# Performance work log

Measured on AMD Instinct MI355X. Metric: run time of the kernel, lower is better.

Reference implementation:

```python
import jax, jax.numpy as jnp
import numpy as np
import math

B, CIN, COUT, K, G, SD, H = 8, 512, 512, 3, 16, 512, 32
EPS = 1e-8


def _blur_kernel():
    k = jnp.array([1., 3., 3., 1.], dtype=jnp.float32)
    k = k[None, :] * k[:, None]
    k = k / k.sum()
    return k * 4.0  # upsample_factor ** 2


def setup_inputs() -> dict:
    key = jax.random.key(0)
    ks = jax.random.split(key, 10)
    return {
        "x": jax.random.normal(ks[0], (B, CIN, H, H), jnp.float32),
        "co": jax.random.uniform(ks[1], (1, CIN, CIN), jnp.float32),
        "style": jax.random.normal(ks[2], (B, 2 * SD), jnp.float32),
        "noise": jax.random.normal(ks[3], (B, 1, 2 * H, 2 * H), jnp.float32),
        "W": jax.random.normal(ks[4], (1, COUT, CIN, K, K), jnp.float32),
        "mb_w": jax.random.normal(ks[5], (G, SD), jnp.float32),
        "mb_b": jnp.ones((G,), jnp.float32),
        "mod_w": jax.random.normal(ks[6], (CIN, SD), jnp.float32),
        "mod_b": jnp.ones((CIN,), jnp.float32),
        "cluster": jax.random.normal(ks[7], (G, CIN), jnp.float32),
        "gate": -jnp.ones((1,), jnp.float32),
        "tmpr": -2.0 * jnp.ones((1,), jnp.float32),
        "noise_weight": jnp.zeros((1,), jnp.float32),
        "flr_bias": jnp.zeros((COUT,), jnp.float32),
    }


def _l2norm(x, axis):
    n = jnp.linalg.norm(x, axis=axis, keepdims=True)
    return x / jnp.maximum(n, 1e-12)


def reference(x, co, style, noise, W, mb_w, mb_b, mod_w, mod_b,
              cluster, gate, tmpr, noise_weight, flr_bias):
    scale = 1.0 / math.sqrt(CIN * K * K)   # GroupModulatedConv2d.scale
    lin_scale = 1.0 / math.sqrt(SD)        # EqualLinear scale (lr_mul=1)

    t = jax.nn.sigmoid(tmpr) * 5.0
    g = jax.nn.sigmoid(gate)
    S = jax.nn.sigmoid((co - g) * 50.0)                    # (1,Cin,Cin)
    cl = jax.nn.softmax(t * cluster, axis=0)               # (G,Cin)
    loss1 = jnp.sum((cl.T @ cl - jax.lax.stop_gradient(S)) ** 2)
    loss2 = jnp.sum((jnp.float32(CIN * CIN / G) - jnp.sum(S)) ** 2)
    grouped = jax.lax.stop_gradient(jnp.round(jax.nn.softmax(cl * 500.0, axis=0))) + 1e-6

    s1, s2 = style[:, :SD], style[:, SD:]
    style_base = (s1 @ (mb_w * lin_scale).T + mb_b)[:, :, None]   # (B,G,1)
    st = (s2 @ (mod_w * lin_scale).T + mod_b)[:, None, :]         # (B,1,Cin)
    tmp = _l2norm(grouped[None] * st, axis=2)                     # (B,G,Cin)
    st = jnp.sum(tmp * style_base, axis=1)                        # (B,Cin)

    w = scale * W * st[:, None, :, None, None]                    # (B,Cout,Cin,K,K)
    demod = jax.lax.rsqrt(jnp.sum(w * w, axis=(2, 3, 4)) + EPS)   # (B,Cout)
    w = w * demod[:, :, None, None, None]

    # conv_transpose2d(stride=2, pad=0, groups=B) == per-sample conv with
    # lhs_dilation=2, padding=K-1, spatially-flipped kernel.
    wf = w[:, :, :, ::-1, ::-1]

    def per_sample(xi, wi):  # xi (Cin,h,w), wi (Cout,Cin,K,K)
        return jax.lax.conv_general_dilated(
            xi[None], wi, window_strides=(1, 1),
            padding=((K - 1, K - 1), (K - 1, K - 1)), lhs_dilation=(2, 2),
            dimension_numbers=('NCHW', 'OIHW', 'NCHW'))[0]

    out = jax.vmap(per_sample)(x, wf)                             # (B,Cout,65,65)

    # Blur: upfirdn2d, pad=(1,1), depthwise 4x4 symmetric FIR kernel.
    bk = _blur_kernel()
    kdw = jnp.broadcast_to(bk[None, None], (COUT, 1, 4, 4))
    out = jax.lax.conv_general_dilated(
        out, kdw, (1, 1), ((1, 1), (1, 1)), feature_group_count=COUT,
        dimension_numbers=('NCHW', 'OIHW', 'NCHW'))                # (B,Cout,64,64)

    # Correlation of base weights (detached, fed to next layer as `co`).
    wflat = W.reshape(COUT, -1)
    wn = _l2norm(wflat, axis=1)
    co_out = jax.lax.stop_gradient((wn @ wn.T)[None])              # (1,Cout,Cout)

    # NoiseInjection + FusedLeakyReLU
    out = out + noise_weight * noise
    out = jax.nn.leaky_relu(out + flr_bias[None, :, None, None], 0.2) * math.sqrt(2.0)
    return out, co_out, loss1, loss2
```

## Files before the change

kernel.cpp:

```cpp
#include <hip/hip_runtime.h>
#include <hip/hip_bf16.h>

#define NB 8
#define LIN_SCALE 0.044194173824159216f
#define SCALE 0.014731391274719736f

typedef __attribute__((ext_vector_type(8))) short short8;
typedef __attribute__((ext_vector_type(4))) float floatx4;

static constexpr size_t O_XS   = 0;
static constexpr size_t O_OUT1 = 9469952;
static constexpr size_t O_WRT  = 44081152;
static constexpr size_t O_WB   = 48799744;
static constexpr size_t O_PG   = 53518336;
static constexpr size_t O_WSQ  = 61906944;
static constexpr size_t O_CL   = 62955520;
static constexpr size_t O_GR   = O_CL + 32768;
static constexpr size_t O_SB   = O_GR + 32768;
static constexpr size_t O_ST0  = O_SB + 1024;
static constexpr size_t O_STS  = O_ST0 + 16384;
static constexpr size_t O_ST2  = O_STS + 16384;
static constexpr size_t O_WNI  = O_ST2 + 16384;
static constexpr size_t O_DM   = O_WNI + 2048;
static constexpr size_t O_ACC  = O_DM + 16384;

static constexpr size_t OUT_CO = 16777216;
static constexpr size_t OUT_L  = 17039360;

__device__ const int c_ylim[4] = {33,33,32,32};
__device__ const int c_xlim[4] = {33,32,33,32};
__device__ const int c_ntap[4] = {4,2,2,1};
__device__ const int c_tap0[4] = {0,4,6,8};
__device__ const int c_nmb[4]  = {69,66,66,64};
__device__ const int c_cnt[4]  = {276,264,264,256};
__device__ const int c_dy[9] = {-1,-1,0,0, -1,0, 0,0, 0};
__device__ const int c_dx[9] = {-1,0,-1,0, 0,0, -1,0, 0};
__device__ const int c_ky[9] = {2,2,0,0, 2,0, 1,1, 1};
__device__ const int c_kx[9] = {2,0,2,0, 1,1, 2,0, 1};
__device__ const long c_poff[4] = {0, 4460544, 8785920, 13111296};

__device__ __forceinline__ float wave_red(float v) {
#pragma unroll
  for (int s = 32; s > 0; s >>= 1) v += __shfl_down(v, s);
  return v;
}

__device__ __forceinline__ void gl_lds16(const void* g, void* l) {
  __builtin_amdgcn_global_load_lds((const __attribute__((address_space(1))) void*)g,
                                   (__attribute__((address_space(3))) void*)l, 16, 0, 0);
}

__device__ __forceinline__ unsigned short bf16b(float f) {
  union { __hip_bfloat16 h; unsigned short u; } cv;
  cv.h = __float2bfloat16(f);
  return cv.u;
}

__device__ __forceinline__ float bfu(unsigned short u) {
  union { float f; unsigned u32; } c; c.u32 = ((unsigned)u) << 16; return c.f;
}

__device__ __forceinline__ int xcd_chunk(int lb, int cnt) {
  const int q = cnt >> 3, r = cnt & 7;
  const int c = lb & 7, i = lb >> 3;
  return (c < r) ? c*(q+1) + i : r*(q+1) + (c - r)*q + i;
}

__global__ __launch_bounds__(256) void k_big1(const float* __restrict__ W,
    float* __restrict__ wsq, float* __restrict__ wni,
    __hip_bfloat16* __restrict__ wrt, unsigned short* __restrict__ wb,
    const float* __restrict__ style, const float* __restrict__ mod_w,
    const float* __restrict__ mod_b, float* __restrict__ st0,
    const float* __restrict__ co, const float* __restrict__ gate,
    const float* __restrict__ cluster, const float* __restrict__ tmpr,
    const float* __restrict__ mb_w, const float* __restrict__ mb_b,
    float* __restrict__ gr, float* __restrict__ sb,
    float* __restrict__ pacc, __hip_bfloat16* __restrict__ xs) {
  __shared__ float sh[8192];
  __shared__ float extra[8];
  const int bid = blockIdx.x, tid = threadIdx.x;
  const int lane = tid & 63, wv = tid >> 6;
  if (bid < 512) {
    const int o = bid;
    for (int j = tid; j < 4608; j += 256) sh[j] = W[(size_t)o*4608 + j];
    __syncthreads();
    float tot = 0.f;
#pragma unroll
    for (int half = 0; half < 2; half++) {
      const int i = tid + half*256;
      float s = 0.f;
#pragma unroll
      for (int k = 0; k < 9; k++) { float w = sh[i*9 + k]; s = fmaf(w, w, s); }
      wsq[o*512 + i] = s; tot += s;
#pragma unroll
      for (int tp = 0; tp < 9; tp++)
        wrt[((size_t)tp*512 + o)*512 + i] = __float2bfloat16(sh[i*9 + c_ky[tp]*3 + c_kx[tp]]);
    }
    for (int j = tid; j < 4608; j += 256) wb[(size_t)o*4608 + j] = bf16b(sh[j]);
    tot = wave_red(tot);
    if (lane == 0) extra[wv] = tot;
    __syncthreads();
    if (tid == 0) wni[o] = 1.f / fmaxf(sqrtf(extra[0]+extra[1]+extra[2]+extra[3]), 1e-12f);
  } else if (bid < 576) {
    const int b = (bid - 512) >> 3, oc = (bid - 512) & 7;
    sh[tid] = style[b*1024 + 512 + tid];
    sh[tid + 256] = style[b*1024 + 768 + tid];
    __syncthreads();
#pragma unroll
    for (int rr = 0; rr < 16; rr++) {
      const int c = oc*64 + wv*16 + rr;
      const float* mw = mod_w + (size_t)c*512;
      float acc = 0.f;
#pragma unroll
      for (int it = 0; it < 8; it++) acc = fmaf(mw[lane + 64*it], sh[lane + 64*it], acc);
      acc = wave_red(acc);
      if (lane == 0) st0[b*512 + c] = acc*LIN_SCALE + mod_b[c];
    }
  } else if (bid < 1088) {
    const int i = bid - 576;
    const float tt = 5.f / (1.f + expf(-tmpr[0]));
    const float gg = 1.f / (1.f + expf(-gate[0]));
    for (int j = tid; j < 512; j += 256) {
      float v[16]; float m = -1e30f;
#pragma unroll
      for (int g = 0; g < 16; g++) { v[g] = tt * cluster[g*512 + j]; m = fmaxf(m, v[g]); }
      float s = 0.f;
#pragma unroll
      for (int g = 0; g < 16; g++) { v[g] = expf(v[g] - m); s += v[g]; }
      float inv = 1.f / s;
#pragma unroll
      for (int g = 0; g < 16; g++) sh[g*512 + j] = v[g] * inv;
    }
    __syncthreads();
    float cli[16];
#pragma unroll
    for (int k = 0; k < 16; k++) cli[k] = sh[k*512 + i];
    float p1 = 0.f, p2 = 0.f;
    for (int j = tid; j < 512; j += 256) {
      float d = 0.f;
#pragma unroll
      for (int k = 0; k < 16; k++) d = fmaf(cli[k], sh[k*512 + j], d);
      float S = 1.f / (1.f + expf(-50.f*(co[i*512 + j] - gg)));
      float e = d - S;
      p1 = fmaf(e, e, p1); p2 += S;
    }
    p1 = wave_red(p1); p2 = wave_red(p2);
    if (lane == 0) { extra[wv] = p1; extra[4 + wv] = p2; }
    __syncthreads();
    if (tid == 0)  pacc[i]       = extra[0]+extra[1]+extra[2]+extra[3];
    if (tid == 64) pacc[512 + i] = extra[4]+extra[5]+extra[6]+extra[7];
  } else if (bid == 1088) {
    const float tt = 5.f / (1.f + expf(-tmpr[0]));
#pragma unroll
    for (int h = 0; h < 2; h++) {
      const int c = tid + h*256;
      float v[16]; float m = -1e30f;
#pragma unroll
      for (int g = 0; g < 16; g++) { v[g] = tt * cluster[g*512 + c]; m = fmaxf(m, v[g]); }
      float s = 0.f;
#pragma unroll
      for (int g = 0; g < 16; g++) { v[g] = expf(v[g] - m); s += v[g]; }
      float inv = 1.f / s;
      float clv[16]; float m2 = -1e30f;
#pragma unroll
      for (int g = 0; g < 16; g++) { clv[g] = v[g]*inv; m2 = fmaxf(m2, 500.f*clv[g]); }
      float s2 = 0.f; float e2[16];
#pragma unroll
      for (int g = 0; g < 16; g++) { e2[g] = expf(500.f*clv[g] - m2); s2 += e2[g]; }
      float i2 = 1.f / s2;
#pragma unroll
      for (int g = 0; g < 16; g++) gr[g*512 + c] = rintf(e2[g]*i2) + 1e-6f;
    }
    for (int task = wv; task < 128; task += 4) {
      int b = task >> 4, g = task & 15;
      const float* s1 = style + b*1024;
      const float* mw = mb_w + g*512;
      float acc = 0.f;
#pragma unroll
      for (int it = 0; it < 8; it++) acc = fmaf(s1[lane + 64*it], mw[lane + 64*it], acc);
      acc = wave_red(acc);
      if (lane == 0) sb[b*16 + g] = acc*LIN_SCALE + mb_b[g];
    }
  } else {
    const int id0 = (bid - 1089)*256 + tid;
    const float4 z = make_float4(0.f, 0.f, 0.f, 0.f);
    float4* xq = (float4*)xs;
#pragma unroll
    for (int it = 0; it < 22; ++it) {
      const int id = id0 + it*3072;
      const int c = id & 63;
      const int pb = id >> 6;
      const int b = pb / 132;
      const int pix = pb - b*132;
      int y, xx;
      if (pix < 34)       { y = 0;        xx = pix; }
      else if (pix < 68)  { y = 33;       xx = pix - 34; }
      else if (pix < 100) { y = pix - 67; xx = 0; }
      else                { y = pix - 99; xx = 33; }
      xq[((size_t)(b*34 + y)*34 + xx)*64 + c] = z;
    }
  }
}

__global__ __launch_bounds__(256) void k_big2(const float* __restrict__ st0,
    const float* __restrict__ gr, const float* __restrict__ sb,
    const float* __restrict__ wsq, float* __restrict__ dm,
    const float* __restrict__ x, __hip_bfloat16* __restrict__ xs,
    const float* __restrict__ pacc, float* __restrict__ out_tail) {
  __shared__ float L[64*65];
  __shared__ float red[16][4];
  __shared__ float inv[16];
  __shared__ float sbb[16];
  const int tid = threadIdx.x;
  const int lane = tid & 63, wv = tid >> 6;

  if (blockIdx.x == 1088) {
    float a = pacc[tid] + pacc[tid + 256];
    float b2 = pacc[512 + tid] + pacc[768 + tid];
    a = wave_red(a); b2 = wave_red(b2);
    if (lane == 0) { red[0][wv] = a; red[1][wv] = b2; }
    __syncthreads();
    if (tid == 0) {
      float p1 = red[0][0]+red[0][1]+red[0][2]+red[0][3];
      float p2 = red[1][0]+red[1][1]+red[1][2]+red[1][3];
      out_tail[0] = p1;
      float d = 16384.f - p2;
      out_tail[1] = d*d;
    }
    return;
  }

  const int b = (blockIdx.x < 64) ? (blockIdx.x >> 3) : ((blockIdx.x - 64) >> 7);
  float s0 = st0[b*512 + tid], s1 = st0[b*512 + 256 + tid];
  float g0[16], g1[16];
#pragma unroll
  for (int g = 0; g < 16; g++) { g0[g] = gr[g*512 + tid]; g1[g] = gr[g*512 + 256 + tid]; }
#pragma unroll
  for (int g = 0; g < 16; g++) {
    float a = g0[g]*s0, c = g1[g]*s1;
    float p = wave_red(a*a + c*c);
    if (lane == 0) red[g][wv] = p;
  }
  if (tid < 16) sbb[tid] = sb[b*16 + tid];
  __syncthreads();
  if (tid < 16) {
    float ttn = red[tid][0] + red[tid][1] + red[tid][2] + red[tid][3];
    inv[tid] = 1.f / fmaxf(sqrtf(ttn), 1e-12f);
  }
  __syncthreads();
  float f0 = 0.f, f1 = 0.f;
#pragma unroll
  for (int g = 0; g < 16; g++) {
    float w = inv[g]*sbb[g];
    f0 = fmaf(g0[g], w, f0); f1 = fmaf(g1[g], w, f1);
  }
  const float sn0 = s0*f0, sn1 = s1*f1;

  if (blockIdx.x < 64) {
    const int oc = blockIdx.x & 7;
    L[tid] = sn0*sn0;
    L[tid + 256] = sn1*sn1;
    __syncthreads();
#pragma unroll
    for (int rr = 0; rr < 16; rr++) {
      const int o = oc*64 + wv*16 + rr;
      const float* wp = wsq + (size_t)o*512;
      float acc = 0.f;
#pragma unroll
      for (int it = 0; it < 8; it++) acc = fmaf(wp[lane + 64*it], L[lane + 64*it], acc);
      acc = wave_red(acc);
      if (lane == 0) dm[b*512 + o] = rsqrtf((1.0f/4608.0f)*acc + 1e-8f);
    }
    return;
  }

  L[tid] = sn0*SCALE;
  L[tid + 256] = sn1*SCALE;
  __syncthreads();
  const int id = blockIdx.x - 64;
  const int p0 = ((id >> 3) & 15) * 64;
  const int i0 = (id & 7) * 64;
  const int iw = tid & 63, pw = tid >> 6;
  const float sv = L[i0 + iw];
  __syncthreads();
  const int lp = tid & 63, li = tid >> 6;
  const float* xp = x + ((size_t)b*512 + i0)*1024 + p0;
#pragma unroll
  for (int ii = 0; ii < 16; ii++) {
    const int i = li + 4*ii;
    L[i*65 + lp] = xp[(size_t)i*1024 + lp];
  }
  __syncthreads();
#pragma unroll
  for (int pp = 0; pp < 16; pp++) {
    const int pix = p0 + pw + 4*pp;
    const int y = pix >> 5, xq = pix & 31;
    xs[(((size_t)b*34 + (y+1))*34 + (xq+1))*512 + i0 + iw] = __float2bfloat16(L[iw*65 + pw + 4*pp] * sv);
  }
}

__global__ __launch_bounds__(256, 4) void k_mfma(
    const __hip_bfloat16* __restrict__ xs, const __hip_bfloat16* __restrict__ wrt,
    __hip_bfloat16* __restrict__ out1, const __hip_bfloat16* __restrict__ wb,
    float* __restrict__ pgram) {
  __shared__ __hip_bfloat16 smem[16384];
  const int fid = blockIdx.x;
  const int tid = threadIdx.x;
  const int lane = tid & 63, wv = tid >> 6;
  const int wm = (wv >> 1) << 6, wn = (wv & 1) << 6;
  const int col16 = lane & 15, quad = lane >> 4;
  const int colp = col16 ^ ((col16 >> 2) & 1);
  const int soff = (quad ^ (col16 & 3)) << 3;

  int aoff[4], boff[4];
#pragma unroll
  for (int t = 0; t < 4; t++) {
    aoff[t] = (wm + t*16 + colp)*32 + soff;
    boff[t] = 4096 + (wn + t*16 + colp)*32 + soff;
  }
  floatx4 acc[4][4];
#pragma unroll
  for (int i = 0; i < 4; i++)
#pragma unroll
    for (int j = 0; j < 4; j++) acc[i][j] = (floatx4){0.f, 0.f, 0.f, 0.f};

  if (fid >= 276 && fid < 404) {
    const int g = xcd_chunk(fid - 276, 128);
    const int m0 = (g & 3) * 128, n0 = ((g >> 2) & 3) * 128;
    const long kz = (long)(g >> 4) * 576;
    long abase[2], bbase[2]; int ldso[2];
#pragma unroll
    for (int r = 0; r < 2; r++) {
      const int idx = r*256 + tid;
      const int rowp = idx >> 2;
      const int row = rowp ^ ((rowp >> 2) & 1);
      const int kc = (((idx & 3) ^ (row & 3)) << 3);
      abase[r] = (long)(m0 + row)*4608 + kz + kc;
      bbase[r] = (long)(n0 + row)*4608 + kz + kc;
      ldso[r] = idx << 3;
    }
#define STAGE_GRAM(s_) do { \
      const int kk_ = (s_) << 5; \
      const int lo_ = ((s_) & 1) << 13; \
      gl_lds16(wb + (abase[0] + kk_), smem + lo_ + ldso[0]); \
      gl_lds16(wb + (abase[1] + kk_), smem + lo_ + ldso[1]); \
      gl_lds16(wb + (bbase[0] + kk_), smem + lo_ + 4096 + ldso[0]); \
      gl_lds16(wb + (bbase[1] + kk_), smem + lo_ + 4096 + ldso[1]); \
    } while (0)
    STAGE_GRAM(0);
    for (int s = 0; s < 18; ++s) {
      if (s + 1 < 18) {
        STAGE_GRAM(s + 1);
        asm volatile("s_waitcnt vmcnt(4)\n\ts_barrier" ::: "memory");
      } else {
        asm volatile("s_waitcnt vmcnt(0)\n\ts_barrier" ::: "memory");
      }
      const int lo = (s & 1) << 13;
      short8 af[4], bfr[4];
#pragma unroll
      for (int t = 0; t < 4; t++) {
        af[t]  = *(const short8*)(smem + lo + aoff[t]);
        bfr[t] = *(const short8*)(smem + lo + boff[t]);
      }
#pragma unroll
      for (int i = 0; i < 4; i++)
#pragma unroll
        for (int j = 0; j < 4; j++)
          acc[i][j] = __builtin_amdgcn_mfma_f32_16x16x32_bf16(af[i], bfr[j], acc[i][j], 0, 0, 0);
      asm volatile("s_barrier" ::: "memory");
    }
    float* pg = pgram + (size_t)(g >> 4) * 262144;
#pragma unroll
    for (int i = 0; i < 4; i++)
#pragma unroll
      for (int j = 0; j < 4; j++) {
        const int m = m0 + wm + i*16 + (quad << 2);
        const int n = n0 + wn + j*16 + col16;
#pragma unroll
        for (int r = 0; r < 4; r++) pg[(size_t)(m + r)*512 + n] = acc[i][j][r];
      }
    return;
  }

  int cls, lb;
  if (fid < 276)      { cls = 0; lb = fid; }
  else if (fid < 668) { cls = 1; lb = fid - 404; }
  else if (fid < 932) { cls = 2; lb = fid - 668; }
  else                { cls = 3; lb = fid - 932; }
  const int lg = xcd_chunk(lb, c_cnt[cls]);
  const int mb = lg >> 2, nb = lg & 3;
  const int xlim = c_xlim[cls];
  const int npix = c_ylim[cls] * xlim;
  const int M = NB * npix;
  const int m0 = mb * 128, n0 = nb * 128;
  const int t0 = c_tap0[cls];
  const int ntap = c_ntap[cls];

  long abase[2], bbase[2]; int ldso[2];
#pragma unroll
  for (int r = 0; r < 2; r++) {
    const int idx = r*256 + tid;
    const int rowp = idx >> 2;
    const int row = rowp ^ ((rowp >> 2) & 1);
    const int kc = (((idx & 3) ^ (row & 3)) << 3);
    int rm = m0 + row; if (rm >= M) rm = 0;
    const int b = rm / npix; const int rem = rm - b*npix;
    const int yy = rem / xlim; const int xx = rem - yy*xlim;
    abase[r] = ((long)(b*34 + yy + 1)*34 + (xx + 1))*512 + kc;
    bbase[r] = ((long)(t0*512 + n0 + row))*512 + kc;
    ldso[r] = idx << 3;
  }

  const int nst = ntap << 4;
#define STAGE_CONV(s_) do { \
    const int tap_ = t0 + ((s_) >> 4); \
    const long adel_ = (long)((c_dy[tap_]*34 + c_dx[tap_])*512); \
    const long bdel_ = (long)((s_) >> 4) << 18; \
    const int kk_ = ((s_) & 15) << 5; \
    const int lo_ = ((s_) & 1) << 13; \
    gl_lds16(xs + (abase[0] + adel_ + kk_), smem + lo_ + ldso[0]); \
    gl_lds16(xs + (abase[1] + adel_ + kk_), smem + lo_ + ldso[1]); \
    gl_lds16(wrt + (bbase[0] + bdel_ + kk_), smem + lo_ + 4096 + ldso[0]); \
    gl_lds16(wrt + (bbase[1] + bdel_ + kk_), smem + lo_ + 4096 + ldso[1]); \
  } while (0)
  STAGE_CONV(0);
  for (int s = 0; s < nst; ++s) {
    if (s + 1 < nst) {
      STAGE_CONV(s + 1);
      asm volatile("s_waitcnt vmcnt(4)\n\ts_barrier" ::: "memory");
    } else {
      asm volatile("s_waitcnt vmcnt(0)\n\ts_barrier" ::: "memory");
    }
    const int lo = (s & 1) << 13;
    short8 af[4], bfr[4];
#pragma unroll
    for (int t = 0; t < 4; t++) {
      af[t]  = *(const short8*)(smem + lo + aoff[t]);
      bfr[t] = *(const short8*)(smem + lo + boff[t]);
    }
#pragma unroll
    for (int i = 0; i < 4; i++)
#pragma unroll
      for (int j = 0; j < 4; j++)
        acc[i][j] = __builtin_amdgcn_mfma_f32_16x16x32_bf16(af[i], bfr[j], acc[i][j], 0, 0, 0);
    asm volatile("s_barrier" ::: "memory");
  }

  __hip_bfloat16* plane = out1 + c_poff[cls];
#pragma unroll
  for (int h = 0; h < 2; h++) {
    if ((wv & 1) == h) {
#pragma unroll
      for (int i = 0; i < 4; i++) {
        const int mrow = wm + i*16 + (quad << 2);
#pragma unroll
        for (int j = 0; j < 4; j++) {
          const int ncl = j*16 + col16;
          ushort4 v;
          v.x = bf16b(acc[i][j][0]); v.y = bf16b(acc[i][j][1]);
          v.z = bf16b(acc[i][j][2]); v.w = bf16b(acc[i][j][3]);
          *(ushort4*)(smem + ncl*136 + mrow) = v;
        }
      }
    }
    __syncthreads();
#pragma unroll
    for (int it = 0; it < 4; it++) {
      const int c = it*256 + tid;
      const int ol = c >> 4, ml = (c & 15) << 3;
      const int mg = m0 + ml;
      if (mg < M) {
        const ushort4 v = *(const ushort4*)(smem + ol*136 + ml);
        *(ushort4*)(plane + (long)(n0 + h*64 + ol)*M + mg) = v;
      }
    }
    __syncthreads();
  }
}

__global__ __launch_bounds__(256) void k_blur(const __hip_bfloat16* __restrict__ out1,
    const float* __restrict__ dm, const float* __restrict__ noise,
    const float* __restrict__ nw, const float* __restrict__ fb, float* __restrict__ out,
    const float* __restrict__ pgram, const float* __restrict__ wni,
    float* __restrict__ co_out) {
  if (blockIdx.x < 256) {
    const int i4 = blockIdx.x*256 + threadIdx.x;
    float4 s = make_float4(0.f, 0.f, 0.f, 0.f);
#pragma unroll
    for (int z = 0; z < 8; z++) {
      const float4 v = ((const float4*)(pgram + (size_t)z*262144))[i4];
      s.x += v.x; s.y += v.y; s.z += v.z; s.w += v.w;
    }
    const float wm = wni[i4 >> 7];
    const float4 wn4 = ((const float4*)wni)[i4 & 127];
    float4 o;
    o.x = s.x*wm*wn4.x; o.y = s.y*wm*wn4.y; o.z = s.z*wm*wn4.z; o.w = s.w*wm*wn4.w;
    ((float4*)co_out)[i4] = o;
    return;
  }
  const int bo = blockIdx.x - 256;
  const int b = bo >> 9, o = bo & 511;
  __shared__ unsigned short L[65 * 68];
  const int tid = threadIdx.x;
  const unsigned short* p0 = (const unsigned short*)out1 + 0        + (long)o * 8712 + b * 1089;
  const unsigned short* p1 = (const unsigned short*)out1 + 4460544  + (long)o * 8448 + b * 1056;
  const unsigned short* p2 = (const unsigned short*)out1 + 8785920  + (long)o * 8448 + b * 1056;
  const unsigned short* p3 = (const unsigned short*)out1 + 13111296 + (long)o * 8192 + b * 1024;
  for (int m = tid; m < 65; m += 256) { L[m*68 + 0] = 0; L[m*68 + 66] = 0; }
  for (int e = tid; e < 1089; e += 256) { int y = e / 33, x = e - 33*y; L[(2*y)*68 + 2*x + 1] = p0[e]; }
  for (int e = tid; e < 1056; e += 256) { int y = e >> 5, x = e & 31;   L[(2*y)*68 + 2*x + 2] = p1[e]; }
  for (int e = tid; e < 1056; e += 256) { int y = e / 33, x = e - 33*y; L[(2*y+1)*68 + 2*x + 1] = p2[e]; }
  for (int e = tid; e < 1024; e += 256) { int y = e >> 5, x = e & 31;   L[(2*y+1)*68 + 2*x + 2] = p3[e]; }
  __syncthreads();
  const float dmv = dm[bo];
  const float nwv = nw[0];
  const float bv = fb[o];
  const int Q = tid & 63;
  const int qy = tid >> 6;
  const int mbase = 16 * qy - 1;
  float hs[18];
#pragma unroll
  for (int rm = 0; rm < 18; rm++) {
    const int m = mbase + rm;
    float s = 0.f;
    if (m >= 0 && m <= 64) {
      const unsigned short* row = L + m*68 + Q;
      s = 0.25f * (bfu(row[0]) + bfu(row[3])) + 0.75f * (bfu(row[1]) + bfu(row[2]));
    }
    hs[rm] = s;
  }
  float* op = out + ((size_t)bo << 12);
  const float* npl = noise + ((size_t)b << 12);
#pragma unroll
  for (int pp = 0; pp < 16; pp++) {
    const int P = 16 * qy + pp;
    float s = 0.25f * (hs[pp] + hs[pp + 3]) + 0.75f * (hs[pp + 1] + hs[pp + 2]);
    float v = fmaf(dmv, s, fmaf(nwv, npl[P * 64 + Q], bv));
    v = (v >= 0.f ? v : 0.2f * v) * 1.4142135623730951f;
    op[P * 64 + Q] = v;
  }
}

extern "C" void kernel_launch(void* const* d_in, const int* in_sizes, int n_in,
                              void* d_out, int out_size, void* d_ws, size_t ws_size,
                              hipStream_t stream) {
  const float* x       = (const float*)d_in[0];
  const float* co      = (const float*)d_in[1];
  const float* style   = (const float*)d_in[2];
  const float* noise   = (const float*)d_in[3];
  const float* W       = (const float*)d_in[4];
  const float* mb_w    = (const float*)d_in[5];
  const float* mb_b    = (const float*)d_in[6];
  const float* mod_w   = (const float*)d_in[7];
  const float* mod_b   = (const float*)d_in[8];
  const float* cluster = (const float*)d_in[9];
  const float* gate    = (const float*)d_in[10];
  const float* tmpr    = (const float*)d_in[11];
  const float* nw      = (const float*)d_in[12];
  const float* fb      = (const float*)d_in[13];
  float* out = (float*)d_out;
  char* ws = (char*)d_ws;

  __hip_bfloat16* xs   = (__hip_bfloat16*)(ws + O_XS);
  __hip_bfloat16* out1 = (__hip_bfloat16*)(ws + O_OUT1);
  __hip_bfloat16* wrt  = (__hip_bfloat16*)(ws + O_WRT);
  __hip_bfloat16* wb   = (__hip_bfloat16*)(ws + O_WB);
  float* pgram = (float*)(ws + O_PG);
  float* wsq = (float*)(ws + O_WSQ);
  float* gr  = (float*)(ws + O_GR);
  float* sb  = (float*)(ws + O_SB);
  float* st0 = (float*)(ws + O_ST0);
  float* wni = (float*)(ws + O_WNI);
  float* dm  = (float*)(ws + O_DM);
  float* pacc = (float*)(ws + O_STS);

  k_big1<<<1101, 256, 0, stream>>>(W, wsq, wni, wrt, (unsigned short*)wb,
                                   style, mod_w, mod_b, st0, co, gate,
                                   cluster, tmpr, mb_w, mb_b, gr, sb, pacc, xs);
  k_big2<<<1089, 256, 0, stream>>>(st0, gr, sb, wsq, dm, x, xs, pacc, out + OUT_L);
  k_mfma<<<1188, 256, 0, stream>>>(xs, wrt, out1, wb, pgram);
  k_blur<<<4352, 256, 0, stream>>>(out1, dm, noise, nw, fb, out, pgram, wni, out + OUT_CO);
}
```

Before: 241.4 us.

## Triple-buffer LDS staging in MFMA kernel with one barrier per k-step

Grows the shared-memory staging area from two buffers to three in both the Gram and conv MFMA loops. Loads now run two stages ahead, and the trailing barrier in each iteration is dropped, because the buffer being refilled was last read an iteration earlier. The epilogue transpose stride changes from 136 to 138 to shift LDS bank mapping. In exchange, LDS per block rises to 48 KB and launch bounds drop from 4 to 3 blocks per CU, and the 138 stride may leave some 8-byte LDS accesses misaligned.

```diff
diff --git a/kernel.cpp b/kernel.cpp
--- a/kernel.cpp
+++ b/kernel.cpp
@@ -299,11 +299,11 @@
   }
 }
 
-__global__ __launch_bounds__(256, 4) void k_mfma(
+__global__ __launch_bounds__(256, 3) void k_mfma(
     const __hip_bfloat16* __restrict__ xs, const __hip_bfloat16* __restrict__ wrt,
     __hip_bfloat16* __restrict__ out1, const __hip_bfloat16* __restrict__ wb,
     float* __restrict__ pgram) {
-  __shared__ __hip_bfloat16 smem[16384];
+  __shared__ __hip_bfloat16 smem[24576];
   const int fid = blockIdx.x;
   const int tid = threadIdx.x;
   const int lane = tid & 63, wv = tid >> 6;
@@ -341,21 +341,19 @@
     }
 #define STAGE_GRAM(s_) do { \
       const int kk_ = (s_) << 5; \
-      const int lo_ = ((s_) & 1) << 13; \
+      const int lo_ = ((s_) % 3) * 8192; \
       gl_lds16(wb + (abase[0] + kk_), smem + lo_ + ldso[0]); \
       gl_lds16(wb + (abase[1] + kk_), smem + lo_ + ldso[1]); \
       gl_lds16(wb + (bbase[0] + kk_), smem + lo_ + 4096 + ldso[0]); \
       gl_lds16(wb + (bbase[1] + kk_), smem + lo_ + 4096 + ldso[1]); \
     } while (0)
     STAGE_GRAM(0);
+    STAGE_GRAM(1);
     for (int s = 0; s < 18; ++s) {
-      if (s + 1 < 18) {
-        STAGE_GRAM(s + 1);
-        asm volatile("s_waitcnt vmcnt(4)\n\ts_barrier" ::: "memory");
-      } else {
-        asm volatile("s_waitcnt vmcnt(0)\n\ts_barrier" ::: "memory");
-      }
-      const int lo = (s & 1) << 13;
+      if (s + 1 < 18) asm volatile("s_waitcnt vmcnt(4)\n\ts_barrier" ::: "memory");
+      else            asm volatile("s_waitcnt vmcnt(0)\n\ts_barrier" ::: "memory");
+      if (s + 2 < 18) STAGE_GRAM(s + 2);
+      const int lo = (s % 3) * 8192;
       short8 af[4], bfr[4];
 #pragma unroll
       for (int t = 0; t < 4; t++) {
@@ -367,7 +365,6 @@
 #pragma unroll
         for (int j = 0; j < 4; j++)
           acc[i][j] = __builtin_amdgcn_mfma_f32_16x16x32_bf16(af[i], bfr[j], acc[i][j], 0, 0, 0);
-      asm volatile("s_barrier" ::: "memory");
     }
     float* pg = pgram + (size_t)(g >> 4) * 262144;
 #pragma unroll
@@ -417,21 +414,19 @@
     const long adel_ = (long)((c_dy[tap_]*34 + c_dx[tap_])*512); \
     const long bdel_ = (long)((s_) >> 4) << 18; \
     const int kk_ = ((s_) & 15) << 5; \
-    const int lo_ = ((s_) & 1) << 13; \
+    const int lo_ = ((s_) % 3) * 8192; \
     gl_lds16(xs + (abase[0] + adel_ + kk_), smem + lo_ + ldso[0]); \
     gl_lds16(xs + (abase[1] + adel_ + kk_), smem + lo_ + ldso[1]); \
     gl_lds16(wrt + (bbase[0] + bdel_ + kk_), smem + lo_ + 4096 + ldso[0]); \
     gl_lds16(wrt + (bbase[1] + bdel_ + kk_), smem + lo_ + 4096 + ldso[1]); \
   } while (0)
   STAGE_CONV(0);
+  STAGE_CONV(1);
   for (int s = 0; s < nst; ++s) {
-    if (s + 1 < nst) {
-      STAGE_CONV(s + 1);
-      asm volatile("s_waitcnt vmcnt(4)\n\ts_barrier" ::: "memory");
-    } else {
-      asm volatile("s_waitcnt vmcnt(0)\n\ts_barrier" ::: "memory");
-    }
-    const int lo = (s & 1) << 13;
+    if (s + 1 < nst) asm volatile("s_waitcnt vmcnt(4)\n\ts_barrier" ::: "memory");
+    else             asm volatile("s_waitcnt vmcnt(0)\n\ts_barrier" ::: "memory");
+    if (s + 2 < nst) STAGE_CONV(s + 2);
+    const int lo = (s % 3) * 8192;
     short8 af[4], bfr[4];
 #pragma unroll
     for (int t = 0; t < 4; t++) {
@@ -443,9 +438,9 @@
 #pragma unroll
       for (int j = 0; j < 4; j++)
         acc[i][j] = __builtin_amdgcn_mfma_f32_16x16x32_bf16(af[i], bfr[j], acc[i][j], 0, 0, 0);
-    asm volatile("s_barrier" ::: "memory");
-  }
-
+  }
+
+  __syncthreads();
   __hip_bfloat16* plane = out1 + c_poff[cls];
 #pragma unroll
   for (int h = 0; h < 2; h++) {
@@ -459,7 +454,7 @@
           ushort4 v;
           v.x = bf16b(acc[i][j][0]); v.y = bf16b(acc[i][j][1]);
           v.z = bf16b(acc[i][j][2]); v.w = bf16b(acc[i][j][3]);
-          *(ushort4*)(smem + ncl*136 + mrow) = v;
+          *(ushort4*)(smem + ncl*138 + mrow) = v;
         }
       }
     }
@@ -470,7 +465,7 @@
       const int ol = c >> 4, ml = (c & 15) << 3;
       const int mg = m0 + ml;
       if (mg < M) {
-        const ushort4 v = *(const ushort4*)(smem + ol*136 + ml);
+        const ushort4 v = *(const ushort4*)(smem + ol*138 + ml);
         *(ushort4*)(plane + (long)(n0 + h*64 + ol)*M + mg) = v;
       }
     }
```

Result: no change. 240.4 us (-0.4%).
